# Performance work log

Hardware: AMD Instinct MI355X
Metric: run time of the kernel (lower is better)

## Reference

```python
import jax, jax.numpy as jnp
import numpy as np

HW = 128  # BEV heatmap size hardcoded in the module

def conv2d(x, w, b, pad):
    y = jax.lax.conv_general_dilated(x, w, (1, 1), [(pad, pad), (pad, pad)],
                                     dimension_numbers=('NCHW', 'OIHW', 'NCHW'))
    return y + b[None, :, None, None]

def setup_inputs() -> dict:
    key = jax.random.key(0)
    ks = jax.random.split(key, 8)
    B, C, N = 4, 64, 4096
    middle_feat_lidar = jax.random.normal(ks[0], (B, C, HW, HW), dtype=jnp.float32)
    voxels_feat_radar = jax.random.normal(ks[1], (N, C), dtype=jnp.float32)
    rcoors = jax.random.randint(ks[2], (N, 4), 0, HW, dtype=jnp.int64)
    rcoors = rcoors.at[:, 0].set(rcoors[:, 0] % B)  # batch index in [0, B)
    rcs = jax.random.uniform(ks[3], (N,), dtype=jnp.float32) * 6.0
    gamma = jnp.array(1.0, dtype=jnp.float32)  # self.rcs_gamma
    # rcs_att: Conv2d(2, C, 1); compress: Conv2d(2C, C, 3, pad=1)
    att_w = jax.random.normal(ks[4], (C, 2, 1, 1), dtype=jnp.float32) * 0.5
    att_b = jnp.zeros((C,), dtype=jnp.float32)
    comp_w = jax.random.normal(ks[5], (C, 2 * C, 3, 3), dtype=jnp.float32) * (1.0 / np.sqrt(2 * C * 9))
    comp_b = jnp.zeros((C,), dtype=jnp.float32)
    return {"middle_feat_lidar": middle_feat_lidar, "voxels_feat_radar": voxels_feat_radar,
            "rcoors": rcoors, "batch_size": B, "rcs": rcs, "gamma": gamma,
            "att_w": att_w, "att_b": att_b, "comp_w": comp_w, "comp_b": comp_b}

def _draw_maps(rcoors, rcs, gamma, batch_size):
    # Vectorized CenterPoint-style gaussian scatter-max over all N points.
    true_rcs = jax.nn.relu(rcs)                      # (N,)
    r = jnp.floor(gamma * true_rcs + 1.0)            # int() truncation; radius >= 1
    sigma = (2.0 * r + 1.0) / 6.0                    # sigma = diameter / 6
    b = rcoors[:, 0]
    y = rcoors[:, 2].astype(jnp.float32)
    x = rcoors[:, 3].astype(jnp.float32)
    grid = jnp.arange(HW, dtype=jnp.float32)
    dy = grid[None, :] - y[:, None]                  # (N, HW) rows
    dx = grid[None, :] - x[:, None]                  # (N, HW) cols
    g = jnp.exp(-(dy[:, :, None] ** 2 + dx[:, None, :] ** 2)
                / (2.0 * sigma[:, None, None] ** 2))  # (N, HW, HW)
    eps = jnp.finfo(jnp.float32).eps
    g = jnp.where(g < eps, 0.0, g)                   # gaussian_2d eps cutoff (max is 1 at center)
    # truncate gaussian to its (2r+1) box, as the slicing in draw_heatmap_gaussian does
    box = (jnp.abs(dy[:, :, None]) <= r[:, None, None]) & (jnp.abs(dx[:, None, :]) <= r[:, None, None])
    g = jnp.where(box, g, 0.0)
    heatmap = jnp.maximum(jax.ops.segment_max(g, b, num_segments=batch_size), 0.0)          # (B,HW,HW)
    heatmap_feat = jnp.maximum(
        jax.ops.segment_max(g * true_rcs[:, None, None], b, num_segments=batch_size), 0.0)  # (B,HW,HW)
    return heatmap, heatmap_feat

def reference(middle_feat_lidar, voxels_feat_radar, rcoors, batch_size, rcs,
              gamma, att_w, att_b, comp_w, comp_b):
    heatmap, heatmap_feat = _draw_maps(rcoors, rcs, gamma, batch_size)
    hm2 = jnp.stack([heatmap, heatmap_feat], axis=1)        # (B,2,HW,HW)
    rcs_features = conv2d(hm2, att_w, att_b, pad=0)          # 1x1 conv
    fused = jnp.concatenate([middle_feat_lidar, rcs_features], axis=1)
    return conv2d(fused, comp_w, comp_b, pad=1)              # 3x3 conv
```

## Files before the change

### kernel.cpp

```cpp
#include <hip/hip_runtime.h>
#include <math.h>

#define HW 128
#define CCH 64

typedef unsigned short u16;
typedef __attribute__((ext_vector_type(8))) short bf16x8;
typedef __attribute__((ext_vector_type(4))) float f32x4;

static __device__ __forceinline__ u16 f2bf(float x) {
    unsigned int u = __float_as_uint(x);
    unsigned int r = (u + 0x7FFFu + ((u >> 16) & 1u)) >> 16;
    return (u16)r;
}

__global__ void prep_kernel(const float* __restrict__ comp_w,
                            const float* __restrict__ att_w,
                            const float* __restrict__ att_b,
                            const int* __restrict__ rcoors,
                            const float* __restrict__ rcs,
                            const float* __restrict__ gamma_p,
                            float* __restrict__ Hm, float* __restrict__ Fm,
                            u16* __restrict__ Wp, int N, int B) {
    __shared__ float part[27][8];
    __shared__ float W3[27];
    int blk = blockIdx.x, tid = threadIdx.x;
    if (blk < 64) {
        int co = blk;
        if (tid < 216) {
            int d = tid >> 3, s = tid & 7;
            int t = d / 3, a = d - t * 3;
            float sum = 0.f;
#pragma unroll
            for (int q = 0; q < 8; ++q) {
                int c2 = s * 8 + q;
                float ww = comp_w[((size_t)co * 128 + 64 + c2) * 9 + t];
                float av = (a == 0) ? att_w[c2 * 2 + 0]
                         : (a == 1) ? att_w[c2 * 2 + 1]
                                    : att_b[c2];
                sum = fmaf(ww, av, sum);
            }
            part[d][s] = sum;
        }
        __syncthreads();
        if (tid < 27) {
            float s = 0.f;
#pragma unroll
            for (int q = 0; q < 8; ++q) s += part[tid][q];
            W3[tid] = s;
        }
        __syncthreads();
        for (int k = tid; k < 672; k += 256) {
            int oct = k >> 3, j = k & 7;
            u16 v = 0;
            if (oct < 81) {
                int t = oct / 9, o = oct - t * 9;
                int ci = o * 8 + j;
                float w = 0.0f;
                if (ci < 64)      w = comp_w[((size_t)co * 128 + ci) * 9 + t];
                else if (ci < 67) w = W3[t * 3 + (ci - 64)];
                v = f2bf(w);
            }
            Wp[co * 672 + k] = v;
        }
    } else {
        int n = blk - 64;
        if (n >= N) return;
        int b  = rcoors[n * 4 + 0];
        int yi = rcoors[n * 4 + 2];
        int xi = rcoors[n * 4 + 3];
        if ((unsigned)b >= (unsigned)B) return;
        float tr = fmaxf(rcs[n], 0.0f);
        float r = floorf(gamma_p[0] * tr + 1.0f);
        float sigma = (2.0f * r + 1.0f) * (1.0f / 6.0f);
        float inv2s2 = 1.0f / (2.0f * sigma * sigma);
        int R = (int)r;
        int W = 2 * R + 1;
        int tot = W * W;
        for (int cell = tid; cell < tot; cell += 256) {
            int cy = cell / W;
            int cx = cell - cy * W;
            int iy = yi - R + cy;
            int ix = xi - R + cx;
            if ((unsigned)iy >= HW || (unsigned)ix >= HW) continue;
            float dy = (float)(iy - yi), dx = (float)(ix - xi);
            float g = expf(-(dy * dy + dx * dx) * inv2s2);
            if (g < 1.1920929e-7f) continue;
            int idx = (b * HW + iy) * HW + ix;
            atomicMax((int*)&Hm[idx], __float_as_int(g));
            float gf = g * tr;
            if (gf > 0.0f) atomicMax((int*)&Fm[idx], __float_as_int(gf));
        }
    }
}

__global__ __launch_bounds__(256)
void conv_kernel(const float* __restrict__ middle,
                 const float* __restrict__ Hm, const float* __restrict__ Fm,
                 const u16* __restrict__ Wp, const float* __restrict__ comp_b,
                 float* __restrict__ out) {
    const int bx = blockIdx.x, by = blockIdx.y, b = blockIdx.z;
    const int tid = threadIdx.x;
    const int wave = tid >> 6, lane = tid & 63;
    const int col = lane & 15, quad = lane >> 4;
    const int i0 = by * 16 - 1, j0 = bx * 16 - 1;

    __shared__ u16 Xs[18 * 18 * 72];

    {
        const float* midB = middle + (size_t)b * CCH * HW * HW;
        const float* HmB = Hm + b * HW * HW;
        const float* FmB = Fm + b * HW * HW;
        for (int u = tid; u < 324 * 9; u += 256) {
            int oct = u / 324, site = u - oct * 324;
            int rr = site / 18, cc = site - rr * 18;
            int gi = i0 + rr, gj = j0 + cc;
            bool in = ((unsigned)gi < HW) && ((unsigned)gj < HW);
            union { u16 h[8]; uint4 v; } pk;
            pk.v = make_uint4(0u, 0u, 0u, 0u);
            if (in) {
                if (oct < 8) {
                    const float* p = midB + (size_t)oct * 8 * HW * HW + gi * HW + gj;
#pragma unroll
                    for (int j = 0; j < 8; ++j)
                        pk.h[j] = f2bf(p[(size_t)j * HW * HW]);
                } else {
                    int q = gi * HW + gj;
                    pk.h[0] = f2bf(HmB[q]);
                    pk.h[1] = f2bf(FmB[q]);
                    pk.h[2] = 0x3F80u;
                }
            }
            *(uint4*)(Xs + site * 72 + oct * 8) = pk.v;
        }
    }
    __syncthreads();

    f32x4 acc[4][4];
#pragma unroll
    for (int m = 0; m < 4; ++m)
#pragma unroll
        for (int n = 0; n < 4; ++n) acc[m][n] = (f32x4){0.f, 0.f, 0.f, 0.f};

#pragma unroll
    for (int c = 0; c < 21; ++c) {
        bf16x8 af[4];
#pragma unroll
        for (int m = 0; m < 4; ++m)
            af[m] = *(const bf16x8*)(Wp + (m * 16 + col) * 672 + c * 32 + quad * 8);

        int oct = c * 4 + quad;
        if (oct > 80) oct = 80;
        int t  = oct / 9;
        int o  = oct - t * 9;
        int dy = t / 3, dx = t - dy * 3;
        const u16* Bb = Xs + ((wave * 4 + dy) * 18 + (col + dx)) * 72 + o * 8;

        bf16x8 bfr[4];
#pragma unroll
        for (int n = 0; n < 4; ++n)
            bfr[n] = *(const bf16x8*)(Bb + n * (18 * 72));

#pragma unroll
        for (int m = 0; m < 4; ++m)
#pragma unroll
            for (int n = 0; n < 4; ++n)
                acc[m][n] = __builtin_amdgcn_mfma_f32_16x16x32_bf16(af[m], bfr[n], acc[m][n], 0, 0, 0);
    }

#pragma unroll
    for (int m = 0; m < 4; ++m) {
        int co0 = m * 16 + quad * 4;
#pragma unroll
        for (int n = 0; n < 4; ++n) {
            int i = by * 16 + wave * 4 + n;
            int j = bx * 16 + col;
            float* o0 = out + (((size_t)(b * 64 + co0) * HW + i) * HW + j);
#pragma unroll
            for (int r = 0; r < 4; ++r)
                o0[(size_t)r * HW * HW] = acc[m][n][r] + comp_b[co0 + r];
        }
    }
}

extern "C" void kernel_launch(void* const* d_in, const int* in_sizes, int n_in,
                              void* d_out, int out_size, void* d_ws, size_t ws_size,
                              hipStream_t stream) {
    const float* middle  = (const float*)d_in[0];
    const int*   rcoors  = (const int*)d_in[2];
    const float* rcs     = (const float*)d_in[4];
    const float* gamma   = (const float*)d_in[5];
    const float* att_w   = (const float*)d_in[6];
    const float* att_b   = (const float*)d_in[7];
    const float* comp_w  = (const float*)d_in[8];
    const float* comp_b  = (const float*)d_in[9];
    float* out = (float*)d_out;

    int B = in_sizes[0] / (CCH * HW * HW);
    int N = in_sizes[4];

    float* Hm = (float*)d_ws;
    float* Fm = Hm + (size_t)B * HW * HW;
    u16*   Wp = (u16*)(Fm + (size_t)B * HW * HW);

    prep_kernel<<<dim3(64 + N), 256, 0, stream>>>(comp_w, att_w, att_b,
                                                  rcoors, rcs, gamma,
                                                  Hm, Fm, Wp, N, B);
    conv_kernel<<<dim3(8, 8, B), 256, 0, stream>>>(middle, Hm, Fm, Wp, comp_b, out);
}
```

Baseline: 107.7 us.

## Fuse gaussian heatmap drawing into conv kernel via per-tile point culling

Removes the global atomicMax scatter of gaussian heatmaps. Each conv tile block now scans all radar points, keeps those whose box overlaps its 18x18 halo in shared memory, and computes the heatmap values per pixel as it builds the tile. This gets rid of the N-block scatter launch and the Hm/Fm round trip through global memory. In exchange, every block reads all N points and adds about 48KB of LDS, which lowers occupancy. The list is also capped at 4096 entries.

```diff
diff --git a/kernel.cpp b/kernel.cpp
--- a/kernel.cpp
+++ b/kernel.cpp
@@ -3,6 +3,7 @@
 
 #define HW 128
 #define CCH 64
+#define EPSF 1.1920929e-7f
 
 typedef unsigned short u16;
 typedef __attribute__((ext_vector_type(8))) short bf16x8;
@@ -17,88 +18,55 @@
 __global__ void prep_kernel(const float* __restrict__ comp_w,
                             const float* __restrict__ att_w,
                             const float* __restrict__ att_b,
-                            const int* __restrict__ rcoors,
-                            const float* __restrict__ rcs,
-                            const float* __restrict__ gamma_p,
-                            float* __restrict__ Hm, float* __restrict__ Fm,
-                            u16* __restrict__ Wp, int N, int B) {
+                            u16* __restrict__ Wp) {
     __shared__ float part[27][8];
     __shared__ float W3[27];
-    int blk = blockIdx.x, tid = threadIdx.x;
-    if (blk < 64) {
-        int co = blk;
-        if (tid < 216) {
-            int d = tid >> 3, s = tid & 7;
-            int t = d / 3, a = d - t * 3;
-            float sum = 0.f;
-#pragma unroll
-            for (int q = 0; q < 8; ++q) {
-                int c2 = s * 8 + q;
-                float ww = comp_w[((size_t)co * 128 + 64 + c2) * 9 + t];
-                float av = (a == 0) ? att_w[c2 * 2 + 0]
-                         : (a == 1) ? att_w[c2 * 2 + 1]
-                                    : att_b[c2];
-                sum = fmaf(ww, av, sum);
-            }
-            part[d][s] = sum;
-        }
-        __syncthreads();
-        if (tid < 27) {
-            float s = 0.f;
-#pragma unroll
-            for (int q = 0; q < 8; ++q) s += part[tid][q];
-            W3[tid] = s;
-        }
-        __syncthreads();
-        for (int k = tid; k < 672; k += 256) {
-            int oct = k >> 3, j = k & 7;
-            u16 v = 0;
-            if (oct < 81) {
-                int t = oct / 9, o = oct - t * 9;
-                int ci = o * 8 + j;
-                float w = 0.0f;
-                if (ci < 64)      w = comp_w[((size_t)co * 128 + ci) * 9 + t];
-                else if (ci < 67) w = W3[t * 3 + (ci - 64)];
-                v = f2bf(w);
-            }
-            Wp[co * 672 + k] = v;
-        }
-    } else {
-        int n = blk - 64;
-        if (n >= N) return;
-        int b  = rcoors[n * 4 + 0];
-        int yi = rcoors[n * 4 + 2];
-        int xi = rcoors[n * 4 + 3];
-        if ((unsigned)b >= (unsigned)B) return;
-        float tr = fmaxf(rcs[n], 0.0f);
-        float r = floorf(gamma_p[0] * tr + 1.0f);
-        float sigma = (2.0f * r + 1.0f) * (1.0f / 6.0f);
-        float inv2s2 = 1.0f / (2.0f * sigma * sigma);
-        int R = (int)r;
-        int W = 2 * R + 1;
-        int tot = W * W;
-        for (int cell = tid; cell < tot; cell += 256) {
-            int cy = cell / W;
-            int cx = cell - cy * W;
-            int iy = yi - R + cy;
-            int ix = xi - R + cx;
-            if ((unsigned)iy >= HW || (unsigned)ix >= HW) continue;
-            float dy = (float)(iy - yi), dx = (float)(ix - xi);
-            float g = expf(-(dy * dy + dx * dx) * inv2s2);
-            if (g < 1.1920929e-7f) continue;
-            int idx = (b * HW + iy) * HW + ix;
-            atomicMax((int*)&Hm[idx], __float_as_int(g));
-            float gf = g * tr;
-            if (gf > 0.0f) atomicMax((int*)&Fm[idx], __float_as_int(gf));
-        }
+    int co = blockIdx.x, tid = threadIdx.x;
+    if (tid < 216) {
+        int d = tid >> 3, s = tid & 7;
+        int t = d / 3, a = d - t * 3;
+        float sum = 0.f;
+#pragma unroll
+        for (int q = 0; q < 8; ++q) {
+            int c2 = s * 8 + q;
+            float ww = comp_w[((size_t)co * 128 + 64 + c2) * 9 + t];
+            float av = (a == 0) ? att_w[c2 * 2 + 0]
+                     : (a == 1) ? att_w[c2 * 2 + 1]
+                                : att_b[c2];
+            sum = fmaf(ww, av, sum);
+        }
+        part[d][s] = sum;
+    }
+    __syncthreads();
+    if (tid < 27) {
+        float s = 0.f;
+#pragma unroll
+        for (int q = 0; q < 8; ++q) s += part[tid][q];
+        W3[tid] = s;
+    }
+    __syncthreads();
+    for (int k = tid; k < 672; k += 256) {
+        int oct = k >> 3, j = k & 7;
+        u16 v = 0;
+        if (oct < 81) {
+            int t = oct / 9, o = oct - t * 9;
+            int ci = o * 8 + j;
+            float w = 0.0f;
+            if (ci < 64)      w = comp_w[((size_t)co * 128 + ci) * 9 + t];
+            else if (ci < 67) w = W3[t * 3 + (ci - 64)];
+            v = f2bf(w);
+        }
+        Wp[co * 672 + k] = v;
     }
 }
 
 __global__ __launch_bounds__(256)
 void conv_kernel(const float* __restrict__ middle,
-                 const float* __restrict__ Hm, const float* __restrict__ Fm,
+                 const int* __restrict__ rcoors,
+                 const float* __restrict__ rcs,
+                 const float* __restrict__ gamma_p,
                  const u16* __restrict__ Wp, const float* __restrict__ comp_b,
-                 float* __restrict__ out) {
+                 float* __restrict__ out, int N) {
     const int bx = blockIdx.x, by = blockIdx.y, b = blockIdx.z;
     const int tid = threadIdx.x;
     const int wave = tid >> 6, lane = tid & 63;
@@ -106,11 +74,40 @@
     const int i0 = by * 16 - 1, j0 = bx * 16 - 1;
 
     __shared__ u16 Xs[18 * 18 * 72];
+    __shared__ int   VP[4096];
+    __shared__ float VI[4096];
+    __shared__ float VT[4096];
+    __shared__ int nv;
+
+    if (tid == 0) nv = 0;
+    __syncthreads();
+
+    {
+        float gam = gamma_p[0];
+        for (int n = tid; n < N; n += 256) {
+            int4 rc = ((const int4*)rcoors)[n];
+            if (rc.x != b) continue;
+            float tr = fmaxf(rcs[n], 0.0f);
+            float r = floorf(gam * tr + 1.0f);
+            int ri = (int)r;
+            int yi = rc.z, xi = rc.w;
+            if (yi + ri < i0 || yi - ri > i0 + 17 ||
+                xi + ri < j0 || xi - ri > j0 + 17) continue;
+            float sigma = (2.0f * r + 1.0f) * (1.0f / 6.0f);
+            float inv2s2 = 1.0f / (2.0f * sigma * sigma);
+            int slot = atomicAdd(&nv, 1);
+            if (slot < 4096) {
+                VP[slot] = yi | (xi << 8) | (ri << 16);
+                VI[slot] = inv2s2;
+                VT[slot] = tr;
+            }
+        }
+    }
+    __syncthreads();
+    const int nvl = min(nv, 4096);
 
     {
         const float* midB = middle + (size_t)b * CCH * HW * HW;
-        const float* HmB = Hm + b * HW * HW;
-        const float* FmB = Fm + b * HW * HW;
         for (int u = tid; u < 324 * 9; u += 256) {
             int oct = u / 324, site = u - oct * 324;
             int rr = site / 18, cc = site - rr * 18;
@@ -125,9 +122,20 @@
                     for (int j = 0; j < 8; ++j)
                         pk.h[j] = f2bf(p[(size_t)j * HW * HW]);
                 } else {
-                    int q = gi * HW + gj;
-                    pk.h[0] = f2bf(HmB[q]);
-                    pk.h[1] = f2bf(FmB[q]);
+                    float Hv = 0.0f, Fv = 0.0f;
+                    for (int v = 0; v < nvl; ++v) {
+                        int pv = VP[v];
+                        int dy = gi - (pv & 0xFF);
+                        int dx = gj - ((pv >> 8) & 0xFF);
+                        int ri = pv >> 16;
+                        if (abs(dy) > ri || abs(dx) > ri) continue;
+                        float g = expf(-(float)(dy * dy + dx * dx) * VI[v]);
+                        if (g < EPSF) continue;
+                        Hv = fmaxf(Hv, g);
+                        Fv = fmaxf(Fv, g * VT[v]);
+                    }
+                    pk.h[0] = f2bf(Hv);
+                    pk.h[1] = f2bf(Fv);
                     pk.h[2] = 0x3F80u;
                 }
             }
@@ -199,12 +207,9 @@
     int B = in_sizes[0] / (CCH * HW * HW);
     int N = in_sizes[4];
 
-    float* Hm = (float*)d_ws;
-    float* Fm = Hm + (size_t)B * HW * HW;
-    u16*   Wp = (u16*)(Fm + (size_t)B * HW * HW);
-
-    prep_kernel<<<dim3(64 + N), 256, 0, stream>>>(comp_w, att_w, att_b,
-                                                  rcoors, rcs, gamma,
-                                                  Hm, Fm, Wp, N, B);
-    conv_kernel<<<dim3(8, 8, B), 256, 0, stream>>>(middle, Hm, Fm, Wp, comp_b, out);
-}
+    u16* Wp = (u16*)d_ws;
+
+    prep_kernel<<<dim3(64), 256, 0, stream>>>(comp_w, att_w, att_b, Wp);
+    conv_kernel<<<dim3(8, 8, B), 256, 0, stream>>>(middle, rcoors, rcs, gamma,
+                                                   Wp, comp_b, out, N);
+}
```

Result: slower. 124.0 us (+15.1%).
